# Optimization experiments

Hardware: AMD Instinct MI355X
Metric: run time of the kernel (lower is better)

Reference implementation:

```python
import jax, jax.numpy as jnp
import numpy as np

D_MODEL = 1024
N_HEADS = 16
HEAD_DIM = D_MODEL // N_HEADS
N_MEM = 16
EPS = 1e-5
ROPE_THETA = 10000.0


def layernorm(x, g, b):
    mu = jnp.mean(x, axis=-1, keepdims=True)
    var = jnp.mean(jnp.square(x - mu), axis=-1, keepdims=True)
    return (x - mu) * jax.lax.rsqrt(var + EPS) * g + b


def rope_cos_sin(seq_len, head_dim, dtype):
    inv_freq = 1.0 / (ROPE_THETA ** (jnp.arange(0, head_dim, 2, dtype=jnp.float32) / head_dim))
    pos = jnp.arange(seq_len, dtype=jnp.float32)
    freqs = pos[:, None] * inv_freq[None, :]            # [S, hd/2]
    emb = jnp.concatenate([freqs, freqs], axis=-1)       # [S, hd]
    return jnp.cos(emb).astype(dtype), jnp.sin(emb).astype(dtype)


def rotate_half(x):
    x1, x2 = jnp.split(x, 2, axis=-1)
    return jnp.concatenate([-x2, x1], axis=-1)


def setup_inputs() -> dict:
    key = jax.random.key(0)
    ks = jax.random.split(key, 8)
    B, T, D = 2, 2048, D_MODEL
    x = jax.random.normal(ks[0], (B, T, D), dtype=jnp.float32)
    memory_tokens = jax.random.normal(ks[1], (1, N_MEM, D), dtype=jnp.float32) * 0.02
    s = 1.0 / np.sqrt(D)
    qkv_w = jax.random.uniform(ks[2], (3 * D, D), minval=-s, maxval=s, dtype=jnp.float32)
    qkv_b = jax.random.uniform(ks[3], (3 * D,), minval=-s, maxval=s, dtype=jnp.float32)
    out_w = jax.random.uniform(ks[4], (D, D), minval=-s, maxval=s, dtype=jnp.float32)
    out_b = jax.random.uniform(ks[5], (D,), minval=-s, maxval=s, dtype=jnp.float32)
    norm_g = jnp.ones((D,), jnp.float32)
    norm_b = jnp.zeros((D,), jnp.float32)
    normm_g = jnp.ones((D,), jnp.float32)
    normm_b = jnp.zeros((D,), jnp.float32)
    return {"x": x, "memory_tokens": memory_tokens, "qkv_w": qkv_w, "qkv_b": qkv_b,
            "out_w": out_w, "out_b": out_b, "norm_g": norm_g, "norm_b": norm_b,
            "normm_g": normm_g, "normm_b": normm_b}


def reference(x, memory_tokens, qkv_w, qkv_b, out_w, out_b, norm_g, norm_b, normm_g, normm_b):
    B, T, D = x.shape
    S = N_MEM + T
    residual = x
    x_norm = layernorm(x, norm_g, norm_b)
    mem = layernorm(jnp.broadcast_to(memory_tokens, (B, N_MEM, D)), normm_g, normm_b)
    xm = jnp.concatenate([mem, x_norm], axis=1)                # [B, S, D]
    qkv = xm @ qkv_w.T + qkv_b                                 # [B, S, 3D]
    qkv = qkv.reshape(B, S, 3, N_HEADS, HEAD_DIM)
    q = jnp.transpose(qkv[:, :, 0], (0, 2, 1, 3))              # [B, H, S, hd]
    k = jnp.transpose(qkv[:, :, 1], (0, 2, 1, 3))
    v = jnp.transpose(qkv[:, :, 2], (0, 2, 1, 3))
    cos, sin = rope_cos_sin(S, HEAD_DIM, x.dtype)              # [S, hd]
    q = q * cos + rotate_half(q) * sin
    k = k * cos + rotate_half(k) * sin
    scale = 1.0 / np.sqrt(HEAD_DIM)
    scores = jnp.einsum("bhqd,bhkd->bhqk", q, k) * scale       # [B, H, S, S]
    causal = jnp.tril(jnp.ones((S, S), dtype=bool))
    scores = jnp.where(causal, scores, jnp.finfo(scores.dtype).min)
    attn = jax.nn.softmax(scores, axis=-1)
    out = jnp.einsum("bhqk,bhkd->bhqd", attn, v)               # [B, H, S, hd]
    out = jnp.transpose(out, (0, 2, 1, 3)).reshape(B, S, D)
    out = out @ out_w.T + out_b
    out = out[:, N_MEM:, :]
    return residual + out
```

## Files before the change

kernel.cpp:

```cpp
#include <hip/hip_runtime.h>
#include <cstdint>


using bf16 = __bf16;
typedef __attribute__((ext_vector_type(8))) __bf16 bf16x8;
typedef __attribute__((ext_vector_type(4))) __bf16 bf16x4;
typedef __attribute__((ext_vector_type(4))) float floatx4;

#define MFMA16(a, b, c) __builtin_amdgcn_mfma_f32_16x16x32_bf16(a, b, c, 0, 0, 0)

constexpr int SV = 2064;
constexpr int SP = 2112;
constexpr float LOG2_THETA = 13.287712379549449f;

__device__ __forceinline__ bool dt_is_bf16(const void* p) {
  return *(const uint32_t*)p == 0x3F803F80u;
}

struct f8 { float v[8]; };

__device__ __forceinline__ f8 load8(const void* p, size_t idx, bool bf) {
  f8 r;
  if (bf) {
    bf16x8 t = *(const bf16x8*)((const bf16*)p + idx);
#pragma unroll
    for (int j = 0; j < 8; ++j) r.v[j] = (float)t[j];
  } else {
    float4 a = *(const float4*)((const float*)p + idx);
    float4 b = *(const float4*)((const float*)p + idx + 4);
    r.v[0] = a.x; r.v[1] = a.y; r.v[2] = a.z; r.v[3] = a.w;
    r.v[4] = b.x; r.v[5] = b.y; r.v[6] = b.z; r.v[7] = b.w;
  }
  return r;
}

__device__ __forceinline__ float ld1(const void* p, size_t idx, bool bf) {
  return bf ? (float)((const bf16*)p)[idx] : ((const float*)p)[idx];
}

__device__ __forceinline__ void load16_to_lds(const bf16* gptr, bf16* lptr) {
  auto* g = reinterpret_cast<const __attribute__((address_space(1))) uint32_t*>(
      reinterpret_cast<uintptr_t>(gptr));
  auto* l = reinterpret_cast<__attribute__((address_space(3))) uint32_t*>(
      reinterpret_cast<uintptr_t>(lptr));
  __builtin_amdgcn_global_load_lds(g, l, 16, 0, 0);
}

__global__ __launch_bounds__(256) void conv_w(
    const void* __restrict__ W, const void* __restrict__ flagp,
    bf16* __restrict__ dst) {
  const bool bf = dt_is_bf16(flagp);
  const size_t i = ((size_t)blockIdx.x * 256 + threadIdx.x) * 8;
  const f8 v = load8(W, i, bf);
  bf16x8 o;
#pragma unroll
  for (int j = 0; j < 8; ++j) o[j] = (bf16)v.v[j];
  *(bf16x8*)&dst[i] = o;
}

__global__ __launch_bounds__(256) void rope_tab(float2* __restrict__ tab) {
  const int i = blockIdx.x * 256 + threadIdx.x;
  const int pos = i >> 5, f = i & 31;
  const float ang = (float)pos * exp2f((float)f * (-LOG2_THETA / 32.0f));
  float c, s;
  sincosf(ang, &c, &s);
  tab[i] = make_float2(c, s);
}

__global__ __launch_bounds__(256) void ln_all(
    const void* __restrict__ x, const void* __restrict__ mem,
    const void* __restrict__ ng, const void* __restrict__ nb,
    const void* __restrict__ mg, const void* __restrict__ mb,
    bf16* __restrict__ mem16, bf16* __restrict__ xln) {
  const bool bf = dt_is_bf16(ng);
  const int t = threadIdx.x, wid = t >> 6, lane = t & 63;
  const int row = blockIdx.x * 4 + wid;
  const void *src, *g, *bb;
  size_t soff;
  bf16* out;
  if (row < 16) {
    src = mem; soff = (size_t)row * 1024; g = mg; bb = mb;
    out = mem16 + (size_t)row * 1024;
  } else {
    src = x; soff = (size_t)(row - 16) * 1024; g = ng; bb = nb;
    out = xln + (size_t)(row - 16) * 1024;
  }
  const f8 v0 = load8(src, soff + lane * 8, bf);
  const f8 v1 = load8(src, soff + 512 + lane * 8, bf);
  float sum = 0.f, sq = 0.f;
#pragma unroll
  for (int j = 0; j < 8; ++j) { sum += v0.v[j]; sq += v0.v[j] * v0.v[j]; }
#pragma unroll
  for (int j = 0; j < 8; ++j) { sum += v1.v[j]; sq += v1.v[j] * v1.v[j]; }
#pragma unroll
  for (int off = 1; off < 64; off <<= 1) {
    sum += __shfl_xor(sum, off);
    sq += __shfl_xor(sq, off);
  }
  const float mu = sum * (1.0f / 1024.0f);
  const float var = sq * (1.0f / 1024.0f) - mu * mu;
  const float rstd = rsqrtf(var + 1e-5f);
  const f8 g0 = load8(g, lane * 8, bf), g1 = load8(g, 512 + lane * 8, bf);
  const f8 b0 = load8(bb, lane * 8, bf), b1 = load8(bb, 512 + lane * 8, bf);
  bf16x8 o0, o1;
#pragma unroll
  for (int j = 0; j < 8; ++j) {
    o0[j] = (bf16)((v0.v[j] - mu) * rstd * g0.v[j] + b0.v[j]);
    o1[j] = (bf16)((v1.v[j] - mu) * rstd * g1.v[j] + b1.v[j]);
  }
  *(bf16x8*)&out[lane * 8] = o0;
  *(bf16x8*)&out[512 + lane * 8] = o1;
}

__global__ __launch_bounds__(256) void gemm0_rope(
    const bf16* __restrict__ mem16, const bf16* __restrict__ xln,
    const bf16* __restrict__ Wqb, const void* __restrict__ bias,
    const void* __restrict__ flagp, const float2* __restrict__ rtab,
    bf16* __restrict__ Qg, bf16* __restrict__ Kg, bf16* __restrict__ Vg) {
  const bool bf = dt_is_bf16(flagp);
  __shared__ bf16 As[128 * 32];
  __shared__ bf16 Bs[128 * 32];
  const int t = threadIdx.x;
  const int row0 = blockIdx.x * 128;
  const int col0 = blockIdx.y * 128;
  const int wid = t >> 6, lane = t & 63, lr = lane & 15, lg = lane >> 4;
  const int wrow = (wid >> 1) * 64, wcol = (wid & 1) * 64;
  floatx4 acc[4][4] = {};

  const bf16* agp[2];
  const bf16* bgp[2];
#pragma unroll
  for (int c = 0; c < 2; ++c) {
    const int tt = c * 256 + t;
    int g = row0 + (tt >> 2);
    if (g > 4127) g = 4127;
    const int b2 = (g >= SV) ? 1 : 0;
    const int s = g - b2 * SV;
    const bf16* ap = (s < 16) ? (mem16 + (size_t)s * 1024)
                              : (xln + ((size_t)(b2 * 2048 + s - 16)) * 1024);
    agp[c] = ap + (tt & 3) * 8;
    bgp[c] = Wqb + (size_t)(col0 + (tt >> 2)) * 1024 + (tt & 3) * 8;
  }

  for (int k0 = 0; k0 < 1024; k0 += 32) {
    __syncthreads();
#pragma unroll
    for (int c = 0; c < 2; ++c) {
      const int tt = c * 256 + t;
      load16_to_lds(agp[c] + k0, &As[(tt & ~63) * 8]);
      load16_to_lds(bgp[c] + k0, &Bs[(tt & ~63) * 8]);
    }
    __syncthreads();
    bf16x8 af[4], bfr[4];
#pragma unroll
    for (int i = 0; i < 4; ++i) {
      af[i] = *(const bf16x8*)&As[(wrow + i * 16 + lr) * 32 + lg * 8];
      bfr[i] = *(const bf16x8*)&Bs[(wcol + i * 16 + lr) * 32 + lg * 8];
    }
#pragma unroll
    for (int mi = 0; mi < 4; ++mi)
#pragma unroll
      for (int ni = 0; ni < 4; ++ni)
        acc[mi][ni] = MFMA16(af[mi], bfr[ni], acc[mi][ni]);
  }

  const int colbase = col0 + wcol;
  const int part = colbase >> 10;
  const int h = (colbase >> 6) & 15;

  if (part == 2) {
#pragma unroll
    for (int mi = 0; mi < 4; ++mi) {
      const int gq = row0 + wrow + mi * 16 + lg * 4;
      if (gq >= 2 * SV) continue;
      const int b2 = (gq >= SV) ? 1 : 0;
      const int pos = gq - b2 * SV;
      const size_t hb = (size_t)(b2 * 16 + h) * 64;
#pragma unroll
      for (int ni = 0; ni < 4; ++ni) {
        const int d = ni * 16 + lr;
        const float bc = ld1(bias, colbase + ni * 16 + lr, bf);
        bf16x4 vv;
#pragma unroll
        for (int r = 0; r < 4; ++r) vv[r] = (bf16)(acc[mi][ni][r] + bc);
        *(bf16x4*)&Vg[(hb + d) * SP + pos] = vv;
      }
    }
  } else {
    bf16* Dst = (part == 0) ? Qg : Kg;
    const float qs = (part == 0) ? 0.125f : 1.0f;
    float bv[4];
#pragma unroll
    for (int a = 0; a < 4; ++a) bv[a] = ld1(bias, colbase + a * 16 + lr, bf);
#pragma unroll
    for (int mi = 0; mi < 4; ++mi) {
#pragma unroll
      for (int r = 0; r < 4; ++r) {
        const int g = row0 + wrow + mi * 16 + lg * 4 + r;
        if (g >= 2 * SV) continue;
        const int b2 = (g >= SV) ? 1 : 0;
        const int pos = g - b2 * SV;
        bf16* drow = Dst + ((size_t)(b2 * 16 + h) * SP + pos) * 64;
#pragma unroll
        for (int a = 0; a < 2; ++a) {
          const float2 cs = rtab[pos * 32 + a * 16 + lr];
          const float vlo = (acc[mi][a][r] + bv[a]) * qs;
          const float vhi = (acc[mi][a + 2][r] + bv[a + 2]) * qs;
          drow[a * 16 + lr] = (bf16)(vlo * cs.x - vhi * cs.y);
          drow[32 + a * 16 + lr] = (bf16)(vhi * cs.x + vlo * cs.y);
        }
      }
    }
  }
}

__global__ __launch_bounds__(256) void flash3(
    const bf16* __restrict__ Qg, const bf16* __restrict__ Kg,
    const bf16* __restrict__ Vg, bf16* __restrict__ attn_out) {
  const int qt = 32 - blockIdx.x;
  const int bh = blockIdx.y;
  const int b = bh >> 4, h = bh & 15;
  const bf16* Qb = Qg + (size_t)bh * SP * 64;
  const bf16* Kb = Kg + (size_t)bh * SP * 64;
  const bf16* Vb = Vg + (size_t)bh * 64 * SP;

  const int t = threadIdx.x;
  const int wid = t >> 6, lane = t & 63, lr = lane & 15, lg = lane >> 4;
  const int qw0 = qt * 64 + wid * 16;

  __shared__ bf16 Ks[64 * 72];
  __shared__ bf16 Vt[64 * 64];
  __shared__ bf16 Ps[4][16 * 72];

  const int qs = qw0 + lr;
  bf16x8 qf0{}, qf1{};
  if (qs < SV) {
    qf0 = *(const bf16x8*)&Qb[(size_t)qs * 64 + lg * 8];
    qf1 = *(const bf16x8*)&Qb[(size_t)qs * 64 + 32 + lg * 8];
  }

  floatx4 o[4] = {};
  float lpart[4] = {};

  const int kr = t >> 2;
  const int kc = (t & 3) * 16;
  const int vd = t >> 2;
  const int vg0 = t & 3;
  const int vswz = ((vd & 7) ^ ((vd >> 4) & 3)) << 3;

  bf16x8 kA, kB, vA, vB;
  kA = *(const bf16x8*)&Kb[(size_t)kr * 64 + kc];
  kB = *(const bf16x8*)&Kb[(size_t)kr * 64 + kc + 8];
  vA = *(const bf16x8*)&Vb[(size_t)vd * SP + vg0 * 8];
  vB = *(const bf16x8*)&Vb[(size_t)vd * SP + (vg0 + 4) * 8];

  for (int kt = 0; kt <= qt; ++kt) {
    const int k0 = kt * 64;
    __syncthreads();
    *(bf16x8*)&Ks[kr * 72 + kc] = kA;
    *(bf16x8*)&Ks[kr * 72 + kc + 8] = kB;
    *(bf16x8*)&Vt[vd * 64 + ((vg0 << 3) ^ vswz)] = vA;
    *(bf16x8*)&Vt[vd * 64 + (((vg0 + 4) << 3) ^ vswz)] = vB;
    __syncthreads();
    if (kt < qt) {
      const int kn = k0 + 64;
      kA = *(const bf16x8*)&Kb[(size_t)(kn + kr) * 64 + kc];
      kB = *(const bf16x8*)&Kb[(size_t)(kn + kr) * 64 + kc + 8];
      vA = *(const bf16x8*)&Vb[(size_t)vd * SP + kn + vg0 * 8];
      vB = *(const bf16x8*)&Vb[(size_t)vd * SP + kn + (vg0 + 4) * 8];
    }

    floatx4 c[4] = {};
#pragma unroll
    for (int j2 = 0; j2 < 4; ++j2) {
      const bf16x8 kfa = *(const bf16x8*)&Ks[(j2 * 16 + lr) * 72 + lg * 8];
      const bf16x8 kfb = *(const bf16x8*)&Ks[(j2 * 16 + lr) * 72 + 32 + lg * 8];
      c[j2] = MFMA16(qf0, kfa, c[j2]);
      c[j2] = MFMA16(qf1, kfb, c[j2]);
    }

    const bool nm = (k0 + 63 > qw0);
#pragma unroll
    for (int r = 0; r < 4; ++r) {
      const int row = qw0 + lg * 4 + r;
      bf16* psr = &Ps[wid][(lg * 4 + r) * 72];
      float ls = 0.f;
#pragma unroll
      for (int j2 = 0; j2 < 4; ++j2) {
        float s = c[j2][r];
        if (nm && (k0 + j2 * 16 + lr > row)) s = -1e30f;
        const float p = __expf(s);
        ls += p;
        psr[j2 * 16 + lr] = (bf16)p;
      }
      lpart[r] += ls;
    }
    asm volatile("s_waitcnt lgkmcnt(0)" ::: "memory");
#pragma unroll
    for (int cc = 0; cc < 2; ++cc) {
      const bf16x8 pf = *(const bf16x8*)&Ps[wid][lr * 72 + cc * 32 + lg * 8];
#pragma unroll
      for (int dt = 0; dt < 4; ++dt) {
        const int key8 = (cc * 32 + lg * 8) ^ ((((lr & 7) ^ dt)) << 3);
        const bf16x8 vf = *(const bf16x8*)&Vt[(dt * 16 + lr) * 64 + key8];
        o[dt] = MFMA16(pf, vf, o[dt]);
      }
    }
  }

#pragma unroll
  for (int r = 0; r < 4; ++r) {
    float l = lpart[r];
    l += __shfl_xor(l, 1);
    l += __shfl_xor(l, 2);
    l += __shfl_xor(l, 4);
    l += __shfl_xor(l, 8);
    const int s = qw0 + lg * 4 + r;
    if (s < 16 || s >= SV) continue;
    const float inv = 1.0f / l;
    const size_t rowoff = ((size_t)(b * 2048 + s - 16)) * 1024 + h * 64;
#pragma unroll
    for (int dt = 0; dt < 4; ++dt)
      attn_out[rowoff + dt * 16 + lr] = (bf16)(o[dt][r] * inv);
  }
}

__global__ __launch_bounds__(256) void gemm1_proj(
    const bf16* __restrict__ A, const bf16* __restrict__ Wob,
    const void* __restrict__ bias, const void* __restrict__ x,
    const void* __restrict__ flagp, void* __restrict__ outp) {
  const bool bf = dt_is_bf16(flagp);
  __shared__ bf16 As[128 * 32];
  __shared__ bf16 Bs[128 * 32];
  const int t = threadIdx.x;
  const int row0 = blockIdx.x * 128;
  const int col0 = blockIdx.y * 128;
  const int wid = t >> 6, lane = t & 63, lr = lane & 15, lg = lane >> 4;
  const int wrow = (wid >> 1) * 64, wcol = (wid & 1) * 64;
  floatx4 acc[4][4] = {};

  const bf16* agp[2];
  const bf16* bgp[2];
#pragma unroll
  for (int c = 0; c < 2; ++c) {
    const int tt = c * 256 + t;
    agp[c] = A + (size_t)(row0 + (tt >> 2)) * 1024 + (tt & 3) * 8;
    bgp[c] = Wob + (size_t)(col0 + (tt >> 2)) * 1024 + (tt & 3) * 8;
  }

  for (int k0 = 0; k0 < 1024; k0 += 32) {
    __syncthreads();
#pragma unroll
    for (int c = 0; c < 2; ++c) {
      const int tt = c * 256 + t;
      load16_to_lds(agp[c] + k0, &As[(tt & ~63) * 8]);
      load16_to_lds(bgp[c] + k0, &Bs[(tt & ~63) * 8]);
    }
    __syncthreads();
    bf16x8 af[4], bfr[4];
#pragma unroll
    for (int i = 0; i < 4; ++i) {
      af[i] = *(const bf16x8*)&As[(wrow + i * 16 + lr) * 32 + lg * 8];
      bfr[i] = *(const bf16x8*)&Bs[(wcol + i * 16 + lr) * 32 + lg * 8];
    }
#pragma unroll
    for (int mi = 0; mi < 4; ++mi)
#pragma unroll
      for (int ni = 0; ni < 4; ++ni)
        acc[mi][ni] = MFMA16(af[mi], bfr[ni], acc[mi][ni]);
  }

#pragma unroll
  for (int mi = 0; mi < 4; ++mi) {
#pragma unroll
    for (int r = 0; r < 4; ++r) {
      const int row = row0 + wrow + mi * 16 + lg * 4 + r;
#pragma unroll
      for (int ni = 0; ni < 4; ++ni) {
        const int col = col0 + wcol + ni * 16 + lr;
        const size_t idx = (size_t)row * 1024 + col;
        const float v = acc[mi][ni][r] + ld1(bias, col, bf) + ld1(x, idx, bf);
        if (bf)
          ((bf16*)outp)[idx] = (bf16)v;
        else
          ((float*)outp)[idx] = v;
      }
    }
  }
}

extern "C" void kernel_launch(void* const* d_in, const int* in_sizes, int n_in,
                              void* d_out, int out_size, void* d_ws, size_t ws_size,
                              hipStream_t stream) {
  const void* x = d_in[0];
  const void* mem = d_in[1];
  const void* qkvw = d_in[2];
  const void* qkvb = d_in[3];
  const void* outw = d_in[4];
  const void* outb = d_in[5];
  const void* ng = d_in[6];
  const void* nb = d_in[7];
  const void* mg = d_in[8];
  const void* mb = d_in[9];

  char* ws = (char*)d_ws;
  bf16* mem16 = (bf16*)(ws);
  bf16* xln = (bf16*)(ws + 32768);
  bf16* Qg = (bf16*)(ws + 8421376);
  bf16* Kg = (bf16*)(ws + 17072128);
  bf16* Vg = (bf16*)(ws + 25722880);
  bf16* Wqb = (bf16*)(ws + 34373632);
  bf16* Wob = (bf16*)(ws + 40665088);
  bf16* attn = xln;
  float2* rtab = (float2*)Wob;

  conv_w<<<1536, 256, 0, stream>>>(qkvw, ng, Wqb);
  ln_all<<<1028, 256, 0, stream>>>(x, mem, ng, nb, mg, mb, mem16, xln);
  rope_tab<<<258, 256, 0, stream>>>(rtab);
  gemm0_rope<<<dim3(33, 24), 256, 0, stream>>>(mem16, xln, Wqb, qkvb, ng, rtab,
                                               Qg, Kg, Vg);
  conv_w<<<512, 256, 0, stream>>>(outw, ng, Wob);
  flash3<<<dim3(33, 32), 256, 0, stream>>>(Qg, Kg, Vg, attn);
  gemm1_proj<<<dim3(32, 8), 256, 0, stream>>>(attn, Wob, outb, x, ng, d_out);
}
```

Baseline: 243.5 us.

## Rewrite QKV GEMM with 256x256 tiles, double-buffered LDS and swizzle

The QKV projection GEMM moves from 128x128 tiles with 256 threads and a single LDS buffer to 256x256 tiles with 512 threads, BK=64, and two LDS stages. Global-to-LDS loads for tile k+2 are issued while MFMAs run on the current tile, with explicit vmcnt waits, barriers and setprio. LDS columns are XOR-swizzled to avoid bank conflicts. The aim is to hide memory latency and raise data reuse; the cost is a grid of only 204 blocks at one block per CU, which may underfill the GPU, plus tail waste from row padding.

```diff
diff --git a/kernel.cpp b/kernel.cpp
--- a/kernel.cpp
+++ b/kernel.cpp
@@ -112,66 +112,103 @@
   *(bf16x8*)&out[512 + lane * 8] = o1;
 }
 
-__global__ __launch_bounds__(256) void gemm0_rope(
+__global__ __launch_bounds__(512, 1) void gemm0_rope(
     const bf16* __restrict__ mem16, const bf16* __restrict__ xln,
     const bf16* __restrict__ Wqb, const void* __restrict__ bias,
     const void* __restrict__ flagp, const float2* __restrict__ rtab,
     bf16* __restrict__ Qg, bf16* __restrict__ Kg, bf16* __restrict__ Vg) {
   const bool bf = dt_is_bf16(flagp);
-  __shared__ bf16 As[128 * 32];
-  __shared__ bf16 Bs[128 * 32];
+  __shared__ bf16 SH[65536];
   const int t = threadIdx.x;
-  const int row0 = blockIdx.x * 128;
-  const int col0 = blockIdx.y * 128;
+  const int row0 = blockIdx.x * 256;
+  const int col0 = blockIdx.y * 256;
   const int wid = t >> 6, lane = t & 63, lr = lane & 15, lg = lane >> 4;
-  const int wrow = (wid >> 1) * 64, wcol = (wid & 1) * 64;
-  floatx4 acc[4][4] = {};
-
-  const bf16* agp[2];
-  const bf16* bgp[2];
-#pragma unroll
-  for (int c = 0; c < 2; ++c) {
-    const int tt = c * 256 + t;
-    int g = row0 + (tt >> 2);
+  const int wm = wid >> 2, wn = wid & 3;
+  const int xorv = (lr & 7) << 3;
+
+  const int coff = (((t & 7) ^ ((t >> 3) & 7)) << 3);
+  const bf16* aptr[4];
+  const bf16* bptr[4];
+#pragma unroll
+  for (int s = 0; s < 4; ++s) {
+    int g = row0 + s * 64 + (t >> 3);
     if (g > 4127) g = 4127;
     const int b2 = (g >= SV) ? 1 : 0;
-    const int s = g - b2 * SV;
-    const bf16* ap = (s < 16) ? (mem16 + (size_t)s * 1024)
-                              : (xln + ((size_t)(b2 * 2048 + s - 16)) * 1024);
-    agp[c] = ap + (tt & 3) * 8;
-    bgp[c] = Wqb + (size_t)(col0 + (tt >> 2)) * 1024 + (tt & 3) * 8;
-  }
-
-  for (int k0 = 0; k0 < 1024; k0 += 32) {
-    __syncthreads();
-#pragma unroll
-    for (int c = 0; c < 2; ++c) {
-      const int tt = c * 256 + t;
-      load16_to_lds(agp[c] + k0, &As[(tt & ~63) * 8]);
-      load16_to_lds(bgp[c] + k0, &Bs[(tt & ~63) * 8]);
-    }
-    __syncthreads();
-    bf16x8 af[4], bfr[4];
-#pragma unroll
-    for (int i = 0; i < 4; ++i) {
-      af[i] = *(const bf16x8*)&As[(wrow + i * 16 + lr) * 32 + lg * 8];
-      bfr[i] = *(const bf16x8*)&Bs[(wcol + i * 16 + lr) * 32 + lg * 8];
-    }
-#pragma unroll
-    for (int mi = 0; mi < 4; ++mi)
+    const int ss = g - b2 * SV;
+    const bf16* ap = (ss < 16) ? (mem16 + (size_t)ss * 1024)
+                               : (xln + ((size_t)(b2 * 2048 + ss - 16)) * 1024);
+    aptr[s] = ap + coff;
+    bptr[s] = Wqb + (size_t)(col0 + s * 64 + (t >> 3)) * 1024 + coff;
+  }
+
+  const int ldsbase = (t & ~63) * 8;
+  auto STAGE = [&](int bufi, int k0) {
+    bf16* Ld = SH + bufi * 32768;
+#pragma unroll
+    for (int s = 0; s < 4; ++s)
+      load16_to_lds(aptr[s] + k0, Ld + s * 4096 + ldsbase);
+#pragma unroll
+    for (int s = 0; s < 4; ++s)
+      load16_to_lds(bptr[s] + k0, Ld + 16384 + s * 4096 + ldsbase);
+  };
+
+  floatx4 acc[8][4] = {};
+  STAGE(0, 0);
+  STAGE(1, 64);
+
+  for (int kt = 0; kt < 16; ++kt) {
+    const int cur = kt & 1;
+    if (kt < 15)
+      asm volatile("s_waitcnt vmcnt(8)" ::: "memory");
+    else
+      asm volatile("s_waitcnt vmcnt(0)" ::: "memory");
+    __builtin_amdgcn_s_barrier();
+    __builtin_amdgcn_sched_barrier(0);
+    const bf16* Ab = SH + cur * 32768;
+    const bf16* Bb = Ab + 16384;
+    bf16x8 a0[8], b0[4], a1[8], b1[4];
+#pragma unroll
+    for (int mi = 0; mi < 8; ++mi)
+      a0[mi] = *(const bf16x8*)&Ab[(wm * 128 + mi * 16 + lr) * 64 + ((lg * 8) ^ xorv)];
+#pragma unroll
+    for (int ni = 0; ni < 4; ++ni)
+      b0[ni] = *(const bf16x8*)&Bb[(wn * 64 + ni * 16 + lr) * 64 + ((lg * 8) ^ xorv)];
+    __builtin_amdgcn_s_setprio(1);
+#pragma unroll
+    for (int mi = 0; mi < 8; ++mi)
 #pragma unroll
       for (int ni = 0; ni < 4; ++ni)
-        acc[mi][ni] = MFMA16(af[mi], bfr[ni], acc[mi][ni]);
-  }
-
-  const int colbase = col0 + wcol;
+        acc[mi][ni] = MFMA16(a0[mi], b0[ni], acc[mi][ni]);
+    __builtin_amdgcn_s_setprio(0);
+#pragma unroll
+    for (int mi = 0; mi < 8; ++mi)
+      a1[mi] = *(const bf16x8*)&Ab[(wm * 128 + mi * 16 + lr) * 64 + ((32 + lg * 8) ^ xorv)];
+#pragma unroll
+    for (int ni = 0; ni < 4; ++ni)
+      b1[ni] = *(const bf16x8*)&Bb[(wn * 64 + ni * 16 + lr) * 64 + ((32 + lg * 8) ^ xorv)];
+    __builtin_amdgcn_sched_barrier(0);
+    asm volatile("s_waitcnt lgkmcnt(0)" ::: "memory");
+    __builtin_amdgcn_s_barrier();
+    __builtin_amdgcn_sched_barrier(0);
+    if (kt < 14) STAGE(cur, (kt + 2) * 64);
+    __builtin_amdgcn_s_setprio(1);
+#pragma unroll
+    for (int mi = 0; mi < 8; ++mi)
+#pragma unroll
+      for (int ni = 0; ni < 4; ++ni)
+        acc[mi][ni] = MFMA16(a1[mi], b1[ni], acc[mi][ni]);
+    __builtin_amdgcn_s_setprio(0);
+  }
+
+  const int colbase = col0 + wn * 64;
   const int part = colbase >> 10;
   const int h = (colbase >> 6) & 15;
+  const int row0w = row0 + wm * 128;
 
   if (part == 2) {
 #pragma unroll
-    for (int mi = 0; mi < 4; ++mi) {
-      const int gq = row0 + wrow + mi * 16 + lg * 4;
+    for (int mi = 0; mi < 8; ++mi) {
+      const int gq = row0w + mi * 16 + lg * 4;
       if (gq >= 2 * SV) continue;
       const int b2 = (gq >= SV) ? 1 : 0;
       const int pos = gq - b2 * SV;
@@ -193,10 +230,10 @@
 #pragma unroll
     for (int a = 0; a < 4; ++a) bv[a] = ld1(bias, colbase + a * 16 + lr, bf);
 #pragma unroll
-    for (int mi = 0; mi < 4; ++mi) {
+    for (int mi = 0; mi < 8; ++mi) {
 #pragma unroll
       for (int r = 0; r < 4; ++r) {
-        const int g = row0 + wrow + mi * 16 + lg * 4 + r;
+        const int g = row0w + mi * 16 + lg * 4 + r;
         if (g >= 2 * SV) continue;
         const int b2 = (g >= SV) ? 1 : 0;
         const int pos = g - b2 * SV;
@@ -417,7 +454,7 @@
   conv_w<<<1536, 256, 0, stream>>>(qkvw, ng, Wqb);
   ln_all<<<1028, 256, 0, stream>>>(x, mem, ng, nb, mg, mb, mem16, xln);
   rope_tab<<<258, 256, 0, stream>>>(rtab);
-  gemm0_rope<<<dim3(33, 24), 256, 0, stream>>>(mem16, xln, Wqb, qkvb, ng, rtab,
+  gemm0_rope<<<dim3(17, 12), 512, 0, stream>>>(mem16, xln, Wqb, qkvb, ng, rtab,
                                                Qg, Kg, Vg);
   conv_w<<<512, 256, 0, stream>>>(outw, ng, Wob);
   flash3<<<dim3(33, 32), 256, 0, stream>>>(Qg, Kg, Vg, attn);
```

Result: faster. 232.0 us (-4.7%).
